# Kernel optimization log

Measured on AMD Instinct MI355X. Metric: run time of the kernel, lower is better.

## Reference

```python
import jax, jax.numpy as jnp
import numpy as np

B, M, N, DC = 32, 4096, 8192, 10
NUM_ITERS = 8
TEMP = 0.01      # smooth_min temperature
ALPHA = 100.0    # smooth_sign sharpness
BIG = 100000000.0


def setup_inputs() -> dict:
    rng = np.random.default_rng(0)
    # regular Tanner graph: each check connects to DC distinct variables
    chk_nbrs = np.argpartition(rng.random((M, N)), DC, axis=1)[:, :DC].astype(np.int32)
    p = rng.uniform(1e-3, 0.05, N)
    prior_llr = np.log((1.0 - p) / p).astype(np.float32)
    gamma = (0.1 * rng.standard_normal(N)).astype(np.float32)
    syndromes = rng.integers(0, 2, size=(B, M)).astype(np.float32)
    return {
        "syndromes": jnp.asarray(syndromes),
        "prior_llr": jnp.asarray(prior_llr),
        "gamma": jnp.asarray(gamma),
        "chk_nbrs": jnp.asarray(chk_nbrs),
    }


def _bp(syndromes, prior_llr, gamma, chk_nbrs):
    b = syndromes.shape[0]
    m, dc = chk_nbrs.shape
    n = prior_llr.shape[0]
    eye = jnp.eye(dc, dtype=bool)                      # (dc, dc)
    syn_sgn = 1.0 - 2.0 * syndromes                    # (b, m)
    var_flat = chk_nbrs.reshape(-1)                    # (m*dc,)

    def check_update(v2c):
        # v2c: (b, m, dc) messages var->check along each check's edge list
        s = jnp.tanh(ALPHA * v2c)                      # smooth_sign
        a = jnp.abs(v2c)
        # leave-one-out product of signs: mask diagonal with 1.0
        prod_excl = jnp.prod(jnp.where(eye, 1.0, s[:, :, None, :]), axis=-1)   # (b, m, dc)
        # leave-one-out smooth_min: mask diagonal with BIG, softmin-weighted sum
        a_m = jnp.where(eye, BIG, a[:, :, None, :])                            # (b, m, dc, dc)
        min_excl = jnp.sum(a_m * jax.nn.softmax(-a_m / TEMP, axis=-1), axis=-1)
        return syn_sgn[:, :, None] * prod_excl * min_excl                      # (b, m, dc)

    def scatter_to_vars(c2v):
        # sum of incoming check->var messages per variable: (b, n)
        return jnp.zeros((b, n), c2v.dtype).at[:, var_flat].add(c2v.reshape(b, -1))

    # initial v2c messages = prior LLR of the source variable
    v2c = jnp.broadcast_to(prior_llr[chk_nbrs], (b, m, dc))

    # iteration 0: no memory term
    c2v = check_update(v2c)
    llrs = scatter_to_vars(c2v) + prior_llr[None, :]
    v2c = llrs[:, chk_nbrs] - c2v

    def step(carry, _):
        v2c, llrs = carry
        c2v = check_update(v2c)
        llrs = scatter_to_vars(c2v) + (1.0 - gamma)[None, :] * prior_llr[None, :] + gamma[None, :] * llrs
        v2c = llrs[:, chk_nbrs] - c2v
        return (v2c, llrs), None

    (_, llrs), _ = jax.lax.scan(jax.checkpoint(step), (v2c, llrs), None, length=NUM_ITERS - 1)
    return llrs


def reference(syndromes, prior_llr, gamma, chk_nbrs):
    return _bp(syndromes, prior_llr, gamma, chk_nbrs)
```

## Files before the change

### kernel.cpp

```cpp
#include <hip/hip_runtime.h>

#define B 32
#define M 4096
#define N 8192
#define DC 10
#define NUM_ITERS 8
#define INV_TEMP 100.0f
#define ALPHA 100.0f
#define NB (N * B)
#define MB (M * B)

__global__ __launch_bounds__(256) void prologue_kernel(
    const float* __restrict__ syn,
    const float* __restrict__ prior,
    const float* __restrict__ gamma,
    float* __restrict__ accumA,
    float* __restrict__ L0,
    float* __restrict__ L1,
    float* __restrict__ syn_t,
    float* __restrict__ pg)
{
    int idx = blockIdx.x * blockDim.x + threadIdx.x;
    if (idx < NB) {
        float p = prior[idx >> 5];
        accumA[idx] = 0.0f;
        L0[idx] = p;
        L1[idx] = p;
    }
    if (idx < MB) {
        int b = idx & 31, m = idx >> 5;
        syn_t[idx] = 1.0f - 2.0f * syn[(size_t)b * M + m];
    }
    if (idx < N) pg[idx] = (1.0f - gamma[idx]) * prior[idx];
}

template <int KIND>
__global__ __launch_bounds__(256) void check_kernel(
    const float* __restrict__ syn_t,
    const float* __restrict__ prior,
    const float* __restrict__ pg,
    const float* __restrict__ gamma,
    const int*   __restrict__ nbrs,
    const float* __restrict__ R,
    float*       __restrict__ W,
    float*       __restrict__ Z,
    const float* __restrict__ Lold,
    float*       __restrict__ Lnew,
    float*       __restrict__ c2v)
{
    int idx = blockIdx.x * blockDim.x + threadIdx.x;
    if (idx >= MB) return;
    const int b = idx & 31;
    const int m = idx >> 5;

    Z[idx] = 0.0f;
    Z[idx + MB] = 0.0f;

    const int* nr = nbrs + m * DC;
    float* c2vp = c2v + (size_t)(m * DC) * B + b;

    int nb[DC];
    #pragma unroll
    for (int i = 0; i < DC; ++i) nb[i] = nr[i];

    float v[DC];
    if (KIND == 0) {
        #pragma unroll
        for (int i = 0; i < DC; ++i) v[i] = prior[nb[i]];
    } else if (KIND == 1) {
        #pragma unroll
        for (int i = 0; i < DC; ++i) {
            int g = nb[i] * B + b;
            float l = R[g] + prior[nb[i]];
            Lnew[g] = l;
            v[i] = l - c2vp[(size_t)i * B];
        }
    } else {
        #pragma unroll
        for (int i = 0; i < DC; ++i) {
            int g = nb[i] * B + b;
            float l = R[g] + pg[nb[i]] + gamma[nb[i]] * Lold[g];
            Lnew[g] = l;
            v[i] = l - c2vp[(size_t)i * B];
        }
    }

    float s[DC], a[DC];
    #pragma unroll
    for (int i = 0; i < DC; ++i) {
        s[i] = tanhf(ALPHA * v[i]);
        a[i] = fabsf(v[i]);
    }

    float min1 = 3.4e38f, min2 = 3.4e38f;
    int am = 0;
    #pragma unroll
    for (int i = 0; i < DC; ++i) {
        if (a[i] < min1) { min2 = min1; min1 = a[i]; am = i; }
        else if (a[i] < min2) { min2 = a[i]; }
    }

    float pre[DC + 1], suf[DC + 1];
    pre[0] = 1.0f;
    #pragma unroll
    for (int i = 0; i < DC; ++i) pre[i + 1] = pre[i] * s[i];
    suf[DC] = 1.0f;
    #pragma unroll
    for (int i = DC - 1; i >= 0; --i) suf[i] = suf[i + 1] * s[i];

    float w[DC];
    float se = 0.0f, sae = 0.0f;
    #pragma unroll
    for (int i = 0; i < DC; ++i) {
        w[i] = expf((min1 - a[i]) * INV_TEMP);
        se  += w[i];
        sae += a[i] * w[i];
    }

    float se2 = 0.0f, sae2 = 0.0f;
    #pragma unroll
    for (int j = 0; j < DC; ++j) {
        float e2 = expf((min2 - a[j]) * INV_TEMP);
        e2 = (j != am) ? e2 : 0.0f;
        se2  += e2;
        sae2 += a[j] * e2;
    }
    float me_am = sae2 / se2;

    float ssgn = syn_t[idx];

    #pragma unroll
    for (int i = 0; i < DC; ++i) {
        float me = (i == am) ? me_am : (sae - a[i] * w[i]) / (se - w[i]);
        float out = ssgn * (pre[i] * suf[i + 1]) * me;
        c2vp[(size_t)i * B] = out;
        atomicAdd(&W[nb[i] * B + b], out);
    }
}

__global__ __launch_bounds__(256) void final_kernel(
    const float* __restrict__ R,
    const float* __restrict__ pg,
    const float* __restrict__ gamma,
    const float* __restrict__ Lold,
    float*       __restrict__ out)
{
    int idx = blockIdx.x * blockDim.x + threadIdx.x;
    if (idx >= NB) return;
    int n = idx & (N - 1);
    int b = idx >> 13;
    int goff = n * B + b;
    out[idx] = R[goff] + pg[n] + gamma[n] * Lold[goff];
}

extern "C" void kernel_launch(void* const* d_in, const int* in_sizes, int n_in,
                              void* d_out, int out_size, void* d_ws, size_t ws_size,
                              hipStream_t stream) {
    const float* syn   = (const float*)d_in[0];
    const float* prior = (const float*)d_in[1];
    const float* gamma = (const float*)d_in[2];
    const int*   nbrs  = (const int*)d_in[3];
    float* out = (float*)d_out;

    float* ws = (float*)d_ws;
    float* A[3] = { ws, ws + NB, ws + 2 * (size_t)NB };
    float* L[2] = { ws + 3 * (size_t)NB, ws + 4 * (size_t)NB };
    float* c2v   = ws + 5 * (size_t)NB;
    float* syn_t = c2v + (size_t)M * DC * B;
    float* pg    = syn_t + MB;

    dim3 blk256(256);
    dim3 pgrid((NB + 255) / 256);
    dim3 cgrid((MB + 255) / 256);

    prologue_kernel<<<pgrid, blk256, 0, stream>>>(syn, prior, gamma, A[0], L[0], L[1], syn_t, pg);

    for (int t = 0; t < NUM_ITERS; ++t) {
        float* Rb = A[(t + 2) % 3];
        float* Wb = A[t % 3];
        float* Zb = A[(t + 1) % 3];
        float* Lo = L[t & 1];
        float* Ln = L[(t + 1) & 1];
        if (t == 0) {
            check_kernel<0><<<cgrid, blk256, 0, stream>>>(syn_t, prior, pg, gamma, nbrs,
                                                          nullptr, Wb, Zb, nullptr, nullptr, c2v);
        } else if (t == 1) {
            check_kernel<1><<<cgrid, blk256, 0, stream>>>(syn_t, prior, pg, gamma, nbrs,
                                                          Rb, Wb, Zb, nullptr, Ln, c2v);
        } else {
            check_kernel<2><<<cgrid, blk256, 0, stream>>>(syn_t, prior, pg, gamma, nbrs,
                                                          Rb, Wb, Zb, Lo, Ln, c2v);
        }
    }
    final_kernel<<<pgrid, blk256, 0, stream>>>(A[1], pg, gamma, L[0], out);
}
```

Measured before the change: 94.35 us.

## Assign one thread per edge with shared-memory exchange in check kernel

```diff
diff --git a/kernel.cpp b/kernel.cpp
--- a/kernel.cpp
+++ b/kernel.cpp
@@ -35,7 +35,7 @@
 }
 
 template <int KIND>
-__global__ __launch_bounds__(256) void check_kernel(
+__global__ __launch_bounds__(320) void check_kernel(
     const float* __restrict__ syn_t,
     const float* __restrict__ prior,
     const float* __restrict__ pg,
@@ -48,94 +48,65 @@
     float*       __restrict__ Lnew,
     float*       __restrict__ c2v)
 {
-    int idx = blockIdx.x * blockDim.x + threadIdx.x;
-    if (idx >= MB) return;
-    const int b = idx & 31;
-    const int m = idx >> 5;
+    __shared__ float sh_s[DC][32];
+    __shared__ float sh_a[DC][32];
 
-    Z[idx] = 0.0f;
-    Z[idx + MB] = 0.0f;
+    const int m   = blockIdx.x;
+    const int tid = threadIdx.x;
+    const int i   = tid >> 5;
+    const int b   = tid & 31;
 
-    const int* nr = nbrs + m * DC;
-    float* c2vp = c2v + (size_t)(m * DC) * B + b;
+    const int nb   = nbrs[m * DC + i];
+    const int goff = nb * B + b;
+    const int eoff = (m * DC + i) * B + b;
 
-    int nb[DC];
-    #pragma unroll
-    for (int i = 0; i < DC; ++i) nb[i] = nr[i];
-
-    float v[DC];
+    float v;
     if (KIND == 0) {
-        #pragma unroll
-        for (int i = 0; i < DC; ++i) v[i] = prior[nb[i]];
+        v = prior[nb];
     } else if (KIND == 1) {
-        #pragma unroll
-        for (int i = 0; i < DC; ++i) {
-            int g = nb[i] * B + b;
-            float l = R[g] + prior[nb[i]];
-            Lnew[g] = l;
-            v[i] = l - c2vp[(size_t)i * B];
-        }
+        float l = R[goff] + prior[nb];
+        Lnew[goff] = l;
+        v = l - c2v[eoff];
     } else {
-        #pragma unroll
-        for (int i = 0; i < DC; ++i) {
-            int g = nb[i] * B + b;
-            float l = R[g] + pg[nb[i]] + gamma[nb[i]] * Lold[g];
-            Lnew[g] = l;
-            v[i] = l - c2vp[(size_t)i * B];
-        }
+        float l = R[goff] + pg[nb] + gamma[nb] * Lold[goff];
+        Lnew[goff] = l;
+        v = l - c2v[eoff];
     }
 
-    float s[DC], a[DC];
+    sh_s[i][b] = tanhf(ALPHA * v);
+    sh_a[i][b] = fabsf(v);
+
+    int gtid = m * 320 + tid;
+    if (gtid < NB) Z[gtid] = 0.0f;
+
+    __syncthreads();
+
+    float sj[DC], aj[DC];
     #pragma unroll
-    for (int i = 0; i < DC; ++i) {
-        s[i] = tanhf(ALPHA * v[i]);
-        a[i] = fabsf(v[i]);
+    for (int j = 0; j < DC; ++j) { sj[j] = sh_s[j][b]; aj[j] = sh_a[j][b]; }
+
+    float prod = 1.0f;
+    float amin = 1e30f;
+    #pragma unroll
+    for (int j = 0; j < DC; ++j) {
+        bool o = (j != i);
+        prod *= o ? sj[j] : 1.0f;
+        amin = fminf(amin, o ? aj[j] : 1e30f);
     }
 
-    float min1 = 3.4e38f, min2 = 3.4e38f;
-    int am = 0;
-    #pragma unroll
-    for (int i = 0; i < DC; ++i) {
-        if (a[i] < min1) { min2 = min1; min1 = a[i]; am = i; }
-        else if (a[i] < min2) { min2 = a[i]; }
-    }
-
-    float pre[DC + 1], suf[DC + 1];
-    pre[0] = 1.0f;
-    #pragma unroll
-    for (int i = 0; i < DC; ++i) pre[i + 1] = pre[i] * s[i];
-    suf[DC] = 1.0f;
-    #pragma unroll
-    for (int i = DC - 1; i >= 0; --i) suf[i] = suf[i + 1] * s[i];
-
-    float w[DC];
     float se = 0.0f, sae = 0.0f;
     #pragma unroll
-    for (int i = 0; i < DC; ++i) {
-        w[i] = expf((min1 - a[i]) * INV_TEMP);
-        se  += w[i];
-        sae += a[i] * w[i];
+    for (int j = 0; j < DC; ++j) {
+        float e = expf((amin - aj[j]) * INV_TEMP);
+        e = (j != i) ? e : 0.0f;
+        se  += e;
+        sae += aj[j] * e;
     }
+    float me = sae / se;
 
-    float se2 = 0.0f, sae2 = 0.0f;
-    #pragma unroll
-    for (int j = 0; j < DC; ++j) {
-        float e2 = expf((min2 - a[j]) * INV_TEMP);
-        e2 = (j != am) ? e2 : 0.0f;
-        se2  += e2;
-        sae2 += a[j] * e2;
-    }
-    float me_am = sae2 / se2;
-
-    float ssgn = syn_t[idx];
-
-    #pragma unroll
-    for (int i = 0; i < DC; ++i) {
-        float me = (i == am) ? me_am : (sae - a[i] * w[i]) / (se - w[i]);
-        float out = ssgn * (pre[i] * suf[i + 1]) * me;
-        c2vp[(size_t)i * B] = out;
-        atomicAdd(&W[nb[i] * B + b], out);
-    }
+    float out = syn_t[m * B + b] * prod * me;
+    c2v[eoff] = out;
+    atomicAdd(&W[goff], out);
 }
 
 __global__ __launch_bounds__(256) void final_kernel(
@@ -171,7 +142,8 @@
 
     dim3 blk256(256);
     dim3 pgrid((NB + 255) / 256);
-    dim3 cgrid((MB + 255) / 256);
+    dim3 cgrid(M);
+    dim3 cblk(320);
 
     prologue_kernel<<<pgrid, blk256, 0, stream>>>(syn, prior, gamma, A[0], L[0], L[1], syn_t, pg);
 
@@ -182,14 +154,14 @@
         float* Lo = L[t & 1];
         float* Ln = L[(t + 1) & 1];
         if (t == 0) {
-            check_kernel<0><<<cgrid, blk256, 0, stream>>>(syn_t, prior, pg, gamma, nbrs,
-                                                          nullptr, Wb, Zb, nullptr, nullptr, c2v);
+            check_kernel<0><<<cgrid, cblk, 0, stream>>>(syn_t, prior, pg, gamma, nbrs,
+                                                        nullptr, Wb, Zb, nullptr, nullptr, c2v);
         } else if (t == 1) {
-            check_kernel<1><<<cgrid, blk256, 0, stream>>>(syn_t, prior, pg, gamma, nbrs,
-                                                          Rb, Wb, Zb, nullptr, Ln, c2v);
+            check_kernel<1><<<cgrid, cblk, 0, stream>>>(syn_t, prior, pg, gamma, nbrs,
+                                                        Rb, Wb, Zb, nullptr, Ln, c2v);
         } else {
-            check_kernel<2><<<cgrid, blk256, 0, stream>>>(syn_t, prior, pg, gamma, nbrs,
-                                                          Rb, Wb, Zb, Lo, Ln, c2v);
+            check_kernel<2><<<cgrid, cblk, 0, stream>>>(syn_t, prior, pg, gamma, nbrs,
+                                                        Rb, Wb, Zb, Lo, Ln, c2v);
         }
     }
     final_kernel<<<pgrid, blk256, 0, stream>>>(A[1], pg, gamma, L[0], out);
```

After: 110.5 us. 17.1% more time.

## Replace atomic scatter with CSR gather in separate variable-node kernel

Applied to the files above, without the earlier changes.

```diff
diff --git a/kernel.cpp b/kernel.cpp
--- a/kernel.cpp
+++ b/kernel.cpp
@@ -9,43 +9,46 @@
 #define ALPHA 100.0f
 #define NB (N * B)
 #define MB (M * B)
-
-__global__ __launch_bounds__(256) void prologue_kernel(
+#define NEDGE (M * DC)
+#define CAP 64
+
+__global__ __launch_bounds__(256) void prologue1_kernel(
     const float* __restrict__ syn,
     const float* __restrict__ prior,
     const float* __restrict__ gamma,
-    float* __restrict__ accumA,
-    float* __restrict__ L0,
-    float* __restrict__ L1,
     float* __restrict__ syn_t,
-    float* __restrict__ pg)
+    float* __restrict__ pg,
+    int*   __restrict__ deg)
 {
     int idx = blockIdx.x * blockDim.x + threadIdx.x;
-    if (idx < NB) {
-        float p = prior[idx >> 5];
-        accumA[idx] = 0.0f;
-        L0[idx] = p;
-        L1[idx] = p;
-    }
     if (idx < MB) {
         int b = idx & 31, m = idx >> 5;
         syn_t[idx] = 1.0f - 2.0f * syn[(size_t)b * M + m];
     }
-    if (idx < N) pg[idx] = (1.0f - gamma[idx]) * prior[idx];
+    if (idx < N) {
+        pg[idx]  = (1.0f - gamma[idx]) * prior[idx];
+        deg[idx] = 0;
+    }
+}
+
+__global__ __launch_bounds__(256) void build_csr_kernel(
+    const int* __restrict__ nbrs,
+    int* __restrict__ deg,
+    int* __restrict__ slots)
+{
+    int e = blockIdx.x * blockDim.x + threadIdx.x;
+    if (e >= NEDGE) return;
+    int nb = nbrs[e];
+    int slot = atomicAdd(&deg[nb], 1);
+    if (slot < CAP) slots[nb * CAP + slot] = e;
 }
 
 template <int KIND>
 __global__ __launch_bounds__(256) void check_kernel(
     const float* __restrict__ syn_t,
     const float* __restrict__ prior,
-    const float* __restrict__ pg,
-    const float* __restrict__ gamma,
     const int*   __restrict__ nbrs,
-    const float* __restrict__ R,
-    float*       __restrict__ W,
-    float*       __restrict__ Z,
-    const float* __restrict__ Lold,
-    float*       __restrict__ Lnew,
+    const float* __restrict__ Lprev,
     float*       __restrict__ c2v)
 {
     int idx = blockIdx.x * blockDim.x + threadIdx.x;
@@ -53,36 +56,17 @@
     const int b = idx & 31;
     const int m = idx >> 5;
 
-    Z[idx] = 0.0f;
-    Z[idx + MB] = 0.0f;
-
     const int* nr = nbrs + m * DC;
     float* c2vp = c2v + (size_t)(m * DC) * B + b;
-
-    int nb[DC];
-    #pragma unroll
-    for (int i = 0; i < DC; ++i) nb[i] = nr[i];
 
     float v[DC];
     if (KIND == 0) {
         #pragma unroll
-        for (int i = 0; i < DC; ++i) v[i] = prior[nb[i]];
-    } else if (KIND == 1) {
-        #pragma unroll
-        for (int i = 0; i < DC; ++i) {
-            int g = nb[i] * B + b;
-            float l = R[g] + prior[nb[i]];
-            Lnew[g] = l;
-            v[i] = l - c2vp[(size_t)i * B];
-        }
+        for (int i = 0; i < DC; ++i) v[i] = prior[nr[i]];
     } else {
         #pragma unroll
-        for (int i = 0; i < DC; ++i) {
-            int g = nb[i] * B + b;
-            float l = R[g] + pg[nb[i]] + gamma[nb[i]] * Lold[g];
-            Lnew[g] = l;
-            v[i] = l - c2vp[(size_t)i * B];
-        }
+        for (int i = 0; i < DC; ++i)
+            v[i] = Lprev[nr[i] * B + b] - c2vp[(size_t)i * B];
     }
 
     float s[DC], a[DC];
@@ -132,25 +116,49 @@
     #pragma unroll
     for (int i = 0; i < DC; ++i) {
         float me = (i == am) ? me_am : (sae - a[i] * w[i]) / (se - w[i]);
-        float out = ssgn * (pre[i] * suf[i + 1]) * me;
-        c2vp[(size_t)i * B] = out;
-        atomicAdd(&W[nb[i] * B + b], out);
-    }
-}
-
-__global__ __launch_bounds__(256) void final_kernel(
-    const float* __restrict__ R,
+        c2vp[(size_t)i * B] = ssgn * (pre[i] * suf[i + 1]) * me;
+    }
+}
+
+template <int VK>
+__global__ __launch_bounds__(256) void var_kernel(
+    const float* __restrict__ prior,
     const float* __restrict__ pg,
     const float* __restrict__ gamma,
-    const float* __restrict__ Lold,
+    const int*   __restrict__ deg,
+    const int*   __restrict__ slots,
+    const float* __restrict__ c2v,
+    const float* __restrict__ Lprev,
+    float*       __restrict__ Lcur,
     float*       __restrict__ out)
 {
     int idx = blockIdx.x * blockDim.x + threadIdx.x;
     if (idx >= NB) return;
-    int n = idx & (N - 1);
-    int b = idx >> 13;
-    int goff = n * B + b;
-    out[idx] = R[goff] + pg[n] + gamma[n] * Lold[goff];
+    const int b = idx & 31;
+    const int n = idx >> 5;
+
+    int d = deg[n];
+    if (d > CAP) d = CAP;
+    const int* sl = slots + n * CAP;
+
+    float acc = 0.0f;
+    for (int j = 0; j < d; ++j) {
+        int e = sl[j];
+        acc += c2v[(size_t)e * B + b];
+    }
+
+    float l;
+    if (VK == 0) {
+        l = acc + prior[n];
+    } else {
+        l = acc + pg[n] + gamma[n] * Lprev[idx];
+    }
+
+    if (VK == 2) {
+        out[(size_t)b * N + n] = l;
+    } else {
+        Lcur[idx] = l;
+    }
 }
 
 extern "C" void kernel_launch(void* const* d_in, const int* in_sizes, int n_in,
@@ -163,34 +171,37 @@
     float* out = (float*)d_out;
 
     float* ws = (float*)d_ws;
-    float* A[3] = { ws, ws + NB, ws + 2 * (size_t)NB };
-    float* L[2] = { ws + 3 * (size_t)NB, ws + 4 * (size_t)NB };
-    float* c2v   = ws + 5 * (size_t)NB;
-    float* syn_t = c2v + (size_t)M * DC * B;
+    float* L[2]  = { ws, ws + NB };
+    float* c2v   = ws + 2 * (size_t)NB;
+    float* syn_t = c2v + (size_t)NEDGE * B;
     float* pg    = syn_t + MB;
-
-    dim3 blk256(256);
-    dim3 pgrid((NB + 255) / 256);
+    int*   deg   = (int*)(pg + N);
+    int*   slots = deg + N;
+
+    dim3 blk(256);
+    dim3 pgrid1((MB + 255) / 256);
+    dim3 egrid((NEDGE + 255) / 256);
     dim3 cgrid((MB + 255) / 256);
-
-    prologue_kernel<<<pgrid, blk256, 0, stream>>>(syn, prior, gamma, A[0], L[0], L[1], syn_t, pg);
+    dim3 vgrid((NB + 255) / 256);
+
+    prologue1_kernel<<<pgrid1, blk, 0, stream>>>(syn, prior, gamma, syn_t, pg, deg);
+    build_csr_kernel<<<egrid, blk, 0, stream>>>(nbrs, deg, slots);
 
     for (int t = 0; t < NUM_ITERS; ++t) {
-        float* Rb = A[(t + 2) % 3];
-        float* Wb = A[t % 3];
-        float* Zb = A[(t + 1) % 3];
-        float* Lo = L[t & 1];
-        float* Ln = L[(t + 1) & 1];
+        float* Lp = L[(t + 1) & 1];
+        float* Lc = L[t & 1];
         if (t == 0) {
-            check_kernel<0><<<cgrid, blk256, 0, stream>>>(syn_t, prior, pg, gamma, nbrs,
-                                                          nullptr, Wb, Zb, nullptr, nullptr, c2v);
-        } else if (t == 1) {
-            check_kernel<1><<<cgrid, blk256, 0, stream>>>(syn_t, prior, pg, gamma, nbrs,
-                                                          Rb, Wb, Zb, nullptr, Ln, c2v);
+            check_kernel<0><<<cgrid, blk, 0, stream>>>(syn_t, prior, nbrs, nullptr, c2v);
+            var_kernel<0><<<vgrid, blk, 0, stream>>>(prior, pg, gamma, deg, slots, c2v,
+                                                     nullptr, Lc, nullptr);
+        } else if (t < NUM_ITERS - 1) {
+            check_kernel<1><<<cgrid, blk, 0, stream>>>(syn_t, prior, nbrs, Lp, c2v);
+            var_kernel<1><<<vgrid, blk, 0, stream>>>(prior, pg, gamma, deg, slots, c2v,
+                                                     Lp, Lc, nullptr);
         } else {
-            check_kernel<2><<<cgrid, blk256, 0, stream>>>(syn_t, prior, pg, gamma, nbrs,
-                                                          Rb, Wb, Zb, Lo, Ln, c2v);
+            check_kernel<1><<<cgrid, blk, 0, stream>>>(syn_t, prior, nbrs, Lp, c2v);
+            var_kernel<2><<<vgrid, blk, 0, stream>>>(prior, pg, gamma, deg, slots, c2v,
+                                                     Lp, nullptr, out);
         }
     }
-    final_kernel<<<pgrid, blk256, 0, stream>>>(A[1], pg, gamma, L[0], out);
-}
+}
```

Measured after the change: 138.8 us. 1.47x slower.
